# Optimization experiments

Measured on AMD Instinct MI355X. Metric: run time of the kernel, lower is better.

Reference implementation:

```python
import jax, jax.numpy as jnp
import numpy as np

OUT_RANGE = 6.0
OUT_SHIFT = -3.0


def setup_inputs() -> dict:
    key = jax.random.key(0)
    ks = jax.random.split(key, 6)
    B, T = 128, 64
    A, V, X = 48, 48, 96
    PF = 128
    fdim = (A + 1) * (V + 1) * (X + 1)  # 232897
    return {
        "audio_h": jax.random.normal(ks[0], (B, T, A), jnp.float32),
        "video_h": jax.random.normal(ks[1], (B, T, V), jnp.float32),
        "text_h": jax.random.normal(ks[2], (B, T, X), jnp.float32),
        "W1": jax.random.normal(ks[3], (fdim, PF), jnp.float32) * 0.002,
        "b1": jnp.zeros((PF,), jnp.float32),
        "W2": jax.random.normal(ks[4], (PF, PF), jnp.float32) * 0.05,
        "b2": jnp.zeros((PF,), jnp.float32),
        "W3": jax.random.normal(ks[5], (PF, 1), jnp.float32) * 0.05,
        "b3": jnp.zeros((1,), jnp.float32),
    }


def reference(audio_h, video_h, text_h, W1, b1, W2, b2, W3, b3):
    B, T, A = audio_h.shape
    V = video_h.shape[-1]
    X = text_h.shape[-1]
    one = jnp.ones((B, T, 1), audio_h.dtype)
    a = jnp.concatenate([one, audio_h], axis=-1)  # [B,T,A+1]
    v = jnp.concatenate([one, video_h], axis=-1)  # [B,T,V+1]
    x = jnp.concatenate([one, text_h], axis=-1)   # [B,T,X+1]
    # per-timestep triple outer product, summed over t.
    # flatten order matches torch: audio slowest, then video, text fastest.
    av = jnp.einsum("bta,btv->btav", a, v).reshape(B, T, (A + 1) * (V + 1))
    fusion = jnp.einsum("btp,btx->bpx", av, x).reshape(B, -1)  # [B,(A+1)(V+1)(X+1)]
    # dropout is identity in eval mode
    h1 = jax.nn.relu(fusion @ W1 + b1)
    h2 = jax.nn.relu(h1 @ W2 + b2)
    out = jax.nn.sigmoid(h2 @ W3 + b3) * OUT_RANGE + OUT_SHIFT  # [B,1] in (-3,3)
    return out
```

## Files before the change

kernel.cpp:

```cpp
#include <hip/hip_runtime.h>


#define B_    128
#define T_    64
#define A1    49
#define V1    49
#define X1    97
#define IJ    2401
#define KTOT  232897
#define FP    232928
#define PF    128
#define KC    512
#define NB2   455

typedef short s8v __attribute__((ext_vector_type(8)));
typedef float f4v __attribute__((ext_vector_type(4)));

__device__ __forceinline__ unsigned short f2bf(float f) {
    union { float f; unsigned u; } v; v.f = f;
    return (unsigned short)((v.u + 0x7FFFu + ((v.u >> 16) & 1u)) >> 16);
}
__device__ __forceinline__ float bf2f(unsigned short h) {
    union { unsigned u; float f; } v; v.u = ((unsigned)h) << 16;
    return v.f;
}

__global__ __launch_bounds__(512) void k1_fusion(
    const float* __restrict__ audio, const float* __restrict__ video,
    const float* __restrict__ text, unsigned short* __restrict__ fusion)
{
    __shared__ float a_s[T_ * A1];
    __shared__ unsigned short v_s[T_ * V1];
    __shared__ unsigned short xT[112 * 72];
    __shared__ unsigned short w_ws[8][1552];

    const int b = blockIdx.y;
    const int bx = blockIdx.x;
    const int tid = threadIdx.x;

    for (int idx = tid; idx < T_ * A1; idx += 512) {
        int t = idx / 49, i = idx - t * 49;
        a_s[idx] = (i == 0) ? 1.0f : audio[(b * T_ + t) * 48 + (i - 1)];
        v_s[idx] = f2bf((i == 0) ? 1.0f : video[(b * T_ + t) * 48 + (i - 1)]);
    }
    for (int idx = tid; idx < T_ * X1; idx += 512) {
        int t = idx / 97, k = idx - t * 97;
        xT[k * 72 + t] = f2bf((k == 0) ? 1.0f : text[(b * T_ + t) * 96 + (k - 1)]);
    }
    for (int idx = tid; idx < 15 * 64; idx += 512) {
        xT[(97 + (idx >> 6)) * 72 + (idx & 63)] = 0;
    }
    if (bx == 0) {
        for (int idx = tid; idx < FP - KTOT; idx += 512)
            fusion[(size_t)b * FP + KTOT + idx] = 0;
    }
    __syncthreads();

    const int wave = tid >> 6, lane = tid & 63;
    const int q = lane >> 4, ln = lane & 15;
    unsigned short* w_s = w_ws[wave];

    for (int it = 0; it < 5; ++it) {
        const int tw = it * 8 + wave;
        if (tw >= 38) break;
        const int tl = bx * 38 + tw;
        if (tl >= 151) break;
        const int ij0 = tl * 16;

        {
            int i = ij0 / 49, j = ij0 - (ij0 / 49) * 49;
            #pragma unroll
            for (int ijl = 0; ijl < 16; ++ijl) {
                unsigned short wv = 0;
                if (ij0 + ijl < IJ)
                    wv = f2bf(a_s[lane * 49 + i] * bf2f(v_s[lane * 49 + j]));
                w_s[ijl * 72 + lane] = wv;
                if (++j == 49) { j = 0; ++i; }
            }
        }
        s8v af0 = *(const s8v*)&w_s[ln * 72 + q * 8];
        s8v af1 = *(const s8v*)&w_s[ln * 72 + 32 + q * 8];

        f4v pacc[7];
        #pragma unroll
        for (int nt = 0; nt < 7; ++nt) {
            s8v bf0 = *(const s8v*)&xT[(nt * 16 + ln) * 72 + q * 8];
            s8v bf1 = *(const s8v*)&xT[(nt * 16 + ln) * 72 + 32 + q * 8];
            f4v acc = {0.f, 0.f, 0.f, 0.f};
            acc = __builtin_amdgcn_mfma_f32_16x16x32_bf16(af0, bf0, acc, 0, 0, 0);
            acc = __builtin_amdgcn_mfma_f32_16x16x32_bf16(af1, bf1, acc, 0, 0, 0);
            pacc[nt] = acc;
        }

        #pragma unroll
        for (int nt = 0; nt < 7; ++nt) {
            int kk = nt * 16 + ln;
            if (kk < X1) {
                #pragma unroll
                for (int r = 0; r < 4; ++r)
                    w_s[(q * 4 + r) * 97 + kk] = f2bf(pacc[nt][r]);
            }
        }
        asm volatile("s_waitcnt lgkmcnt(0)" ::: "memory");
        __builtin_amdgcn_sched_barrier(0);

        const int nv = min(16, IJ - ij0);
        const int bytes = nv * 194;
        char* gdst = (char*)(fusion + (size_t)b * FP + (size_t)ij0 * 97);
        const char* lsrc = (const char*)w_s;
        for (int off = lane * 16; off < bytes; off += 1024) {
            uint4 d = *(const uint4*)(lsrc + off);
            *(uint4*)(gdst + off) = d;
        }
    }
}

#define BPAD 40
__global__ __launch_bounds__(512) void k2_gemm(
    const unsigned short* __restrict__ fusion, const float* __restrict__ W1,
    float* __restrict__ partials)
{
    __shared__ unsigned short B_l[2][128 * BPAD];

    const int blk = blockIdx.x;
    const int kbase = blk * KC;
    const int tid = threadIdx.x;
    const int wave = tid >> 6, lane = tid & 63;
    const int q = lane >> 4, ln = lane & 15;
    const int fB = tid & 127, g = tid >> 7;

    const unsigned short* Arow =
        fusion + (size_t)(wave * 16 + ln) * FP + kbase + q * 8;

    f4v acc[8];
    #pragma unroll
    for (int n = 0; n < 8; ++n) acc[n] = (f4v){0.f, 0.f, 0.f, 0.f};

#define LOADW(dst, s)                                                       \
    {                                                                       \
        _Pragma("unroll")                                                   \
        for (int c = 0; c < 8; ++c) {                                       \
            int p = kbase + (s) * 32 + g * 8 + c;                           \
            dst[c] = (p < KTOT) ? W1[(size_t)p * PF + fB] : 0.f;            \
        }                                                                   \
    }
#define PACKW(src, buf)                                                     \
    {                                                                       \
        ushort4 lo, hi;                                                     \
        lo.x = f2bf(src[0]); lo.y = f2bf(src[1]);                           \
        lo.z = f2bf(src[2]); lo.w = f2bf(src[3]);                           \
        hi.x = f2bf(src[4]); hi.y = f2bf(src[5]);                           \
        hi.z = f2bf(src[6]); hi.w = f2bf(src[7]);                           \
        *(ushort4*)&B_l[buf][fB * BPAD + g * 8]     = lo;                   \
        *(ushort4*)&B_l[buf][fB * BPAD + g * 8 + 4] = hi;                   \
    }
#define MFMA8(av, buf)                                                      \
    {                                                                       \
        _Pragma("unroll")                                                   \
        for (int nt = 0; nt < 8; ++nt) {                                    \
            s8v bfv = *(const s8v*)&B_l[buf][(nt * 16 + ln) * BPAD + q * 8];\
            acc[nt] = __builtin_amdgcn_mfma_f32_16x16x32_bf16(              \
                av, bfv, acc[nt], 0, 0, 0);                                 \
        }                                                                   \
    }

    float w0[8], w1[8];
    s8v a0v, a1v;

    LOADW(w0, 0);
    PACKW(w0, 0);
    LOADW(w1, 1);
    a0v = *(const s8v*)Arow;
    __syncthreads();

    for (int i = 0; i < 8; ++i) {
        const bool more = (i < 7);
        if (more) LOADW(w0, 2 * i + 2);
        a1v = *(const s8v*)(Arow + (2 * i + 1) * 32);
        MFMA8(a0v, 0);
        PACKW(w1, 1);
        __syncthreads();
        if (more) {
            LOADW(w1, 2 * i + 3);
            a0v = *(const s8v*)(Arow + (2 * i + 2) * 32);
        }
        MFMA8(a1v, 1);
        if (more) {
            PACKW(w0, 0);
            __syncthreads();
        }
    }
#undef LOADW
#undef PACKW
#undef MFMA8

    float* outp = partials + (size_t)blk * (128 * 128);
    #pragma unroll
    for (int nt = 0; nt < 8; ++nt) {
        const int f = nt * 16 + ln;
        #pragma unroll
        for (int r = 0; r < 4; ++r)
            outp[(wave * 16 + q * 4 + r) * 128 + f] = acc[nt][r];
    }
}

__global__ __launch_bounds__(512) void k3_reduce(
    const float* __restrict__ partials, const float* __restrict__ b1,
    float* __restrict__ h1)
{
    __shared__ float red[512];
    const int e = blockIdx.x * 64 + (threadIdx.x & 63);
    const int rh = threadIdx.x >> 6;
    float s = 0.f;
    for (int r = rh; r < NB2; r += 8)
        s += partials[(size_t)r * 16384 + e];
    red[threadIdx.x] = s;
    __syncthreads();
    if (threadIdx.x < 64) {
        float v = 0.f;
        #pragma unroll
        for (int j = 0; j < 8; ++j) v += red[threadIdx.x + 64 * j];
        v += b1[e & 127];
        h1[e] = fmaxf(v, 0.f);
    }
}

__global__ __launch_bounds__(128) void k4_out(
    const float* __restrict__ h1, const float* __restrict__ W2,
    const float* __restrict__ b2, const float* __restrict__ W3,
    const float* __restrict__ b3, float* __restrict__ out)
{
    __shared__ float hrow[128];
    __shared__ float red2[2];
    const int b = blockIdx.x, f = threadIdx.x;
    hrow[f] = h1[b * 128 + f];
    __syncthreads();
    float s = b2[f];
    #pragma unroll 8
    for (int c = 0; c < 128; ++c) s += hrow[c] * W2[c * 128 + f];
    float p = fmaxf(s, 0.f) * W3[f];
    #pragma unroll
    for (int off = 32; off; off >>= 1) p += __shfl_down(p, off, 64);
    if ((f & 63) == 0) red2[f >> 6] = p;
    __syncthreads();
    if (f == 0) {
        float t = red2[0] + red2[1] + b3[0];
        out[b] = 6.0f / (1.0f + expf(-t)) - 3.0f;
    }
}

extern "C" void kernel_launch(void* const* d_in, const int* in_sizes, int n_in,
                              void* d_out, int out_size, void* d_ws, size_t ws_size,
                              hipStream_t stream)
{
    const float* audio = (const float*)d_in[0];
    const float* video = (const float*)d_in[1];
    const float* text  = (const float*)d_in[2];
    const float* W1 = (const float*)d_in[3];
    const float* b1 = (const float*)d_in[4];
    const float* W2 = (const float*)d_in[5];
    const float* b2 = (const float*)d_in[6];
    const float* W3 = (const float*)d_in[7];
    const float* b3 = (const float*)d_in[8];
    float* out = (float*)d_out;

    char* ws = (char*)d_ws;
    unsigned short* fusion = (unsigned short*)ws;
    float* partials = (float*)(ws + 59629568);
    float* h1 = (float*)(ws + 89448448);

    k1_fusion<<<dim3(4, 128), 512, 0, stream>>>(audio, video, text, fusion);
    k2_gemm<<<dim3(NB2), 512, 0, stream>>>(fusion, W1, partials);
    k3_reduce<<<dim3(256), 512, 0, stream>>>(partials, b1, h1);
    k4_out<<<dim3(128), 128, 0, stream>>>(h1, W2, b2, W3, b3, out);
}
```

Before: 257.4 us.

## Enlarge GEMM K-chunk to one block wave and fuse partial reduction into head

The split-K GEMM now gives each block 928 K-elements instead of 512. That makes 251 blocks, roughly one wave across the CUs, and roughly halves the number of partial-sum tiles written and read back. The separate reduce kernel is removed: the final MLP kernel now sums the partials for its batch row, applies bias and ReLU, and runs the remaining layers, which saves a launch and the h1 round trip. The risk is that the reduction now runs on only 128 blocks, so it has less parallelism for reading the partials.

```diff
diff --git a/kernel.cpp b/kernel.cpp
--- a/kernel.cpp
+++ b/kernel.cpp
@@ -10,8 +10,8 @@
 #define KTOT  232897
 #define FP    232928
 #define PF    128
-#define KC    512
-#define NB2   455
+#define KC2   928
+#define NBLK  251
 
 typedef short s8v __attribute__((ext_vector_type(8)));
 typedef float f4v __attribute__((ext_vector_type(4)));
@@ -123,7 +123,7 @@
     __shared__ unsigned short B_l[2][128 * BPAD];
 
     const int blk = blockIdx.x;
-    const int kbase = blk * KC;
+    const int kbase = blk * KC2;
     const int tid = threadIdx.x;
     const int wave = tid >> 6, lane = tid & 63;
     const int q = lane >> 4, ln = lane & 15;
@@ -173,23 +173,19 @@
     a0v = *(const s8v*)Arow;
     __syncthreads();
 
-    for (int i = 0; i < 8; ++i) {
-        const bool more = (i < 7);
-        if (more) LOADW(w0, 2 * i + 2);
+    for (int i = 0; i < 14; ++i) {
+        LOADW(w0, 2 * i + 2);
         a1v = *(const s8v*)(Arow + (2 * i + 1) * 32);
         MFMA8(a0v, 0);
         PACKW(w1, 1);
         __syncthreads();
-        if (more) {
-            LOADW(w1, 2 * i + 3);
-            a0v = *(const s8v*)(Arow + (2 * i + 2) * 32);
-        }
+        if (i < 13) LOADW(w1, 2 * i + 3);
+        a0v = *(const s8v*)(Arow + (2 * i + 2) * 32);
         MFMA8(a1v, 1);
-        if (more) {
-            PACKW(w0, 0);
-            __syncthreads();
-        }
-    }
+        PACKW(w0, 0);
+        __syncthreads();
+    }
+    MFMA8(a0v, 0);
 #undef LOADW
 #undef PACKW
 #undef MFMA8
@@ -204,46 +200,38 @@
     }
 }
 
-__global__ __launch_bounds__(512) void k3_reduce(
+__global__ __launch_bounds__(256) void k4_out(
     const float* __restrict__ partials, const float* __restrict__ b1,
-    float* __restrict__ h1)
-{
-    __shared__ float red[512];
-    const int e = blockIdx.x * 64 + (threadIdx.x & 63);
-    const int rh = threadIdx.x >> 6;
-    float s = 0.f;
-    for (int r = rh; r < NB2; r += 8)
-        s += partials[(size_t)r * 16384 + e];
-    red[threadIdx.x] = s;
-    __syncthreads();
-    if (threadIdx.x < 64) {
-        float v = 0.f;
-        #pragma unroll
-        for (int j = 0; j < 8; ++j) v += red[threadIdx.x + 64 * j];
-        v += b1[e & 127];
-        h1[e] = fmaxf(v, 0.f);
-    }
-}
-
-__global__ __launch_bounds__(128) void k4_out(
-    const float* __restrict__ h1, const float* __restrict__ W2,
-    const float* __restrict__ b2, const float* __restrict__ W3,
-    const float* __restrict__ b3, float* __restrict__ out)
-{
+    const float* __restrict__ W2, const float* __restrict__ b2,
+    const float* __restrict__ W3, const float* __restrict__ b3,
+    float* __restrict__ out)
+{
+    __shared__ float red[256];
     __shared__ float hrow[128];
     __shared__ float red2[2];
-    const int b = blockIdx.x, f = threadIdx.x;
-    hrow[f] = h1[b * 128 + f];
-    __syncthreads();
-    float s = b2[f];
-    #pragma unroll 8
-    for (int c = 0; c < 128; ++c) s += hrow[c] * W2[c * 128 + f];
-    float p = fmaxf(s, 0.f) * W3[f];
-    #pragma unroll
-    for (int off = 32; off; off >>= 1) p += __shfl_down(p, off, 64);
-    if ((f & 63) == 0) red2[f >> 6] = p;
-    __syncthreads();
-    if (f == 0) {
+    const int b = blockIdx.x, tid = threadIdx.x;
+    const int f = tid & 127, rh = tid >> 7;
+
+    float s = 0.f;
+    #pragma unroll 4
+    for (int r = rh; r < NBLK; r += 2)
+        s += partials[(size_t)r * 16384 + b * 128 + f];
+    red[tid] = s;
+    __syncthreads();
+    if (tid < 128)
+        hrow[f] = fmaxf(red[f] + red[f + 128] + b1[f], 0.f);
+    __syncthreads();
+    if (tid < 128) {
+        float s2 = b2[f];
+        #pragma unroll 8
+        for (int c = 0; c < 128; ++c) s2 += hrow[c] * W2[c * 128 + f];
+        float p = fmaxf(s2, 0.f) * W3[f];
+        #pragma unroll
+        for (int off = 32; off; off >>= 1) p += __shfl_down(p, off, 64);
+        if ((f & 63) == 0) red2[f >> 6] = p;
+    }
+    __syncthreads();
+    if (tid == 0) {
         float t = red2[0] + red2[1] + b3[0];
         out[b] = 6.0f / (1.0f + expf(-t)) - 3.0f;
     }
@@ -267,10 +255,8 @@
     char* ws = (char*)d_ws;
     unsigned short* fusion = (unsigned short*)ws;
     float* partials = (float*)(ws + 59629568);
-    float* h1 = (float*)(ws + 89448448);
 
     k1_fusion<<<dim3(4, 128), 512, 0, stream>>>(audio, video, text, fusion);
-    k2_gemm<<<dim3(NB2), 512, 0, stream>>>(fusion, W1, partials);
-    k3_reduce<<<dim3(256), 512, 0, stream>>>(partials, b1, h1);
-    k4_out<<<dim3(128), 128, 0, stream>>>(h1, W2, b2, W3, b3, out);
-}
+    k2_gemm<<<dim3(NBLK), 512, 0, stream>>>(fusion, W1, partials);
+    k4_out<<<dim3(128), 256, 0, stream>>>(partials, b1, W2, b2, W3, b3, out);
+}
```

Measured after the change: 247.5 us. 1.04x faster.
